# Performance work log

Hardware: AMD Instinct MI355X
Metric: run time of the kernel (lower is better)

Reference implementation:

```python
import jax, jax.numpy as jnp
import numpy as np
import math

D_MODEL = 1024
N_HEADS = 16
D_K = D_MODEL // N_HEADS
B, T = 4, 2048


def setup_inputs() -> dict:
    key = jax.random.key(0)
    ks = jax.random.split(key, 5)
    s = 1.0 / math.sqrt(D_MODEL)
    return {
        "x": jax.random.normal(ks[0], (B, T, D_MODEL), dtype=jnp.float32),
        "W_qkv": jax.random.normal(ks[1], (3 * D_MODEL, D_MODEL), dtype=jnp.float32) * s,
        "b_qkv": jax.random.normal(ks[2], (3 * D_MODEL,), dtype=jnp.float32) * 0.01,
        "W_out": jax.random.normal(ks[3], (D_MODEL, D_MODEL), dtype=jnp.float32) * s,
        "b_out": jax.random.normal(ks[4], (D_MODEL,), dtype=jnp.float32) * 0.01,
    }


def reference(x, W_qkv, b_qkv, W_out, b_out):
    Bn, Tn, C = x.shape
    # qkv projection: [B,T,3C]
    qkv = jnp.einsum("btc,oc->bto", x, W_qkv) + b_qkv
    # NOTE: original reshapes to (B,T,H,3*d_k) THEN chunks -> per-head interleaved layout
    qkv = qkv.reshape(Bn, Tn, N_HEADS, 3 * D_K).transpose(0, 2, 1, 3)  # [B,H,T,3dk]
    q, k, v = jnp.split(qkv, 3, axis=-1)  # each [B,H,T,dk]
    scores = jnp.einsum("bhtd,bhsd->bhts", q, k) / math.sqrt(D_K)
    causal = jnp.tril(jnp.ones((Tn, Tn), dtype=bool))
    scores = jnp.where(causal[None, None], scores, -jnp.inf)
    attn = jax.nn.softmax(scores, axis=-1)
    ctx = jnp.einsum("bhts,bhsd->bhtd", attn, v)  # [B,H,T,dk]
    ctx = ctx.transpose(0, 2, 1, 3).reshape(Bn, Tn, C)
    return jnp.einsum("btc,oc->bto", ctx, W_out) + b_out
```

## Files before the change

### kernel.cpp

```cpp
#include <hip/hip_runtime.h>

typedef __attribute__((ext_vector_type(8))) short short8;
typedef __attribute__((ext_vector_type(4))) float f32x4;
typedef __attribute__((ext_vector_type(16))) float f32x16;
typedef __attribute__((ext_vector_type(4))) unsigned int u32x4;
typedef __attribute__((ext_vector_type(4))) unsigned short u16x4;
typedef unsigned int u32;
typedef unsigned short u16;

#define DEV static __device__ __forceinline__

DEV u16 f2bf(float f) {
  union { float f; u32 u; } c; c.f = f;
  u32 r = (c.u + 0x7fffu + ((c.u >> 16) & 1u)) >> 16;
  return (u16)r;
}
DEV float bf2f(u16 v) {
  union { u32 u; float f; } c; c.u = ((u32)v) << 16;
  return c.f;
}
DEV short8 pack8(float4 a, float4 b) {
  short8 r;
  r[0]=(short)f2bf(a.x); r[1]=(short)f2bf(a.y); r[2]=(short)f2bf(a.z); r[3]=(short)f2bf(a.w);
  r[4]=(short)f2bf(b.x); r[5]=(short)f2bf(b.y); r[6]=(short)f2bf(b.z); r[7]=(short)f2bf(b.w);
  return r;
}
DEV u32 cvtpk(float lo, float hi) {
  u32 r;
  asm("v_cvt_pk_bf16_f32 %0, %1, %2" : "=v"(r) : "v"(lo), "v"(hi));
  return r;
}

#if __has_builtin(__builtin_amdgcn_exp2f)
DEV float fexp2(float x) { return __builtin_amdgcn_exp2f(x); }
#else
DEV float fexp2(float x) { return exp2f(x); }
#endif

DEV void glds16(const void* g, void* l) {
  __builtin_amdgcn_global_load_lds((const __attribute__((address_space(1))) u32*)g,
                                   (__attribute__((address_space(3))) u32*)l, 16, 0, 0);
}

DEV f32x16 mfma32(short8 a, short8 b, f32x16 c) {
  return __builtin_amdgcn_mfma_f32_32x32x16_bf16(a, b, c, 0, 0, 0);
}

constexpr int CDIM = 1024, TT = 2048, NH = 16, DK = 64;
#define QSC 0.1803368801111601f

__global__ void conv_bf16(const float* __restrict__ X, const float* __restrict__ W1,
                          const float* __restrict__ W2, u16* __restrict__ Xb,
                          u16* __restrict__ W1b, u16* __restrict__ W2b) {
  const long n0 = 1048576, n1 = 393216, n2 = 131072;
  for (long i = (long)blockIdx.x * blockDim.x + threadIdx.x; i < n0 + n1 + n2;
       i += (long)gridDim.x * blockDim.x) {
    const float* s; u16* d; long j = i;
    if (j < n0) { s = X; d = Xb; }
    else if (j < n0 + n1) { j -= n0; s = W1; d = W1b; }
    else { j -= n0 + n1; s = W2; d = W2b; }
    float4 a = ((const float4*)s)[2 * j];
    float4 b = ((const float4*)s)[2 * j + 1];
    ((short8*)d)[j] = pack8(a, b);
  }
}

__global__ void __launch_bounds__(512, 2)
qkv_gemm5(const u16* __restrict__ A, const u16* __restrict__ B,
          const float* __restrict__ bias, u16* __restrict__ Qb,
          u16* __restrict__ Kb, u16* __restrict__ VTb) {
  __shared__ u16 LS[3][3][128][64];
  const int tid = threadIdx.x, lane = tid & 63, wid = tid >> 6;
  const int lo = lane & 15, lg = lane >> 4;
  const int wm = wid >> 1, wn = wid & 1;
  const int rin = lane >> 3, blk = lane & 7;
  const int m0 = blockIdx.x * 256, n0 = blockIdx.y * 128;
  const int r7 = lo & 7;

  const u16* gA = A + (size_t)(m0 + wid * 16 + rin) * CDIM + (blk ^ rin) * 8;
  const u16* gB = B + (size_t)(n0 + wid * 16 + rin) * CDIM + (blk ^ rin) * 8;
  u16* lsb = &LS[0][0][wid * 16][0];

#define STGH0(bufi, kt)                                          \
  {                                                              \
    const int k0e = (kt) * 64;                                   \
    u16* lb = lsb + (bufi) * 24576;                              \
    glds16(gA + k0e, lb);                                        \
    glds16(gA + k0e + 8 * CDIM, lb + 512);                       \
    glds16(gB + k0e, lb + 16384);                                \
  }
#define STGH1(bufi, kt)                                          \
  {                                                              \
    const int k0e = (kt) * 64;                                   \
    u16* lb = lsb + (bufi) * 24576;                              \
    glds16(gA + k0e + 128 * CDIM, lb + 8192);                    \
    glds16(gA + k0e + 136 * CDIM, lb + 8704);                    \
    glds16(gB + k0e + 8 * CDIM, lb + 16896);                     \
  }

  f32x4 acc[4][4];
  const f32x4 fz = {0.f, 0.f, 0.f, 0.f};
#pragma unroll
  for (int i = 0; i < 4; ++i)
#pragma unroll
    for (int j = 0; j < 4; ++j) acc[i][j] = fz;

  STGH0(0, 0); STGH1(0, 0);
  STGH0(1, 1); STGH1(1, 1);
  asm volatile("s_waitcnt vmcnt(6)" ::: "memory");
  __builtin_amdgcn_s_barrier();

  int b0 = 0, b1 = 1, b2 = 2;
  for (int T = 0; T < 16; ++T) {
    const u16* pA = &LS[b0][wm >> 1][(wm & 1) * 64][0];
    const u16* pB = &LS[b0][2][wn * 64][0];
    short8 af[4], bfr[4];
#pragma unroll
    for (int mi = 0; mi < 4; ++mi)
      af[mi] = *(const short8*)&pA[(mi * 16 + lo) * 64 + ((lg ^ r7) * 8)];
#pragma unroll
    for (int ni = 0; ni < 4; ++ni)
      bfr[ni] = *(const short8*)&pB[(ni * 16 + lo) * 64 + ((lg ^ r7) * 8)];
    if (T < 14) STGH0(b2, T + 2);
    __builtin_amdgcn_sched_barrier(0);
    __builtin_amdgcn_s_barrier();
    asm volatile("s_waitcnt lgkmcnt(0)" ::: "memory");
    __builtin_amdgcn_sched_barrier(0);
    __builtin_amdgcn_s_setprio(1);
#pragma unroll
    for (int mi = 0; mi < 4; ++mi)
#pragma unroll
      for (int ni = 0; ni < 4; ++ni)
        acc[mi][ni] = __builtin_amdgcn_mfma_f32_16x16x32_bf16(af[mi], bfr[ni], acc[mi][ni], 0, 0, 0);
    __builtin_amdgcn_s_setprio(0);
    __builtin_amdgcn_sched_barrier(0);
    __builtin_amdgcn_s_barrier();
#pragma unroll
    for (int mi = 0; mi < 4; ++mi)
      af[mi] = *(const short8*)&pA[(mi * 16 + lo) * 64 + (((4 + lg) ^ r7) * 8)];
#pragma unroll
    for (int ni = 0; ni < 4; ++ni)
      bfr[ni] = *(const short8*)&pB[(ni * 16 + lo) * 64 + (((4 + lg) ^ r7) * 8)];
    if (T < 14) STGH1(b2, T + 2);
    __builtin_amdgcn_sched_barrier(0);
    if (T < 14) {
      asm volatile("s_waitcnt vmcnt(6)" ::: "memory");
    } else if (T == 14) {
      asm volatile("s_waitcnt vmcnt(0)" ::: "memory");
    }
    __builtin_amdgcn_s_barrier();
    asm volatile("s_waitcnt lgkmcnt(0)" ::: "memory");
    __builtin_amdgcn_sched_barrier(0);
    __builtin_amdgcn_s_setprio(1);
#pragma unroll
    for (int mi = 0; mi < 4; ++mi)
#pragma unroll
      for (int ni = 0; ni < 4; ++ni)
        acc[mi][ni] = __builtin_amdgcn_mfma_f32_16x16x32_bf16(af[mi], bfr[ni], acc[mi][ni], 0, 0, 0);
    __builtin_amdgcn_s_setprio(0);
    __builtin_amdgcn_sched_barrier(0);
    __builtin_amdgcn_s_barrier();
    const int tmp = b0; b0 = b1; b1 = b2; b2 = tmp;
  }
#undef STGH0
#undef STGH1

#pragma unroll
  for (int ni = 0; ni < 4; ++ni) {
    const int o = n0 + wn * 64 + ni * 16 + lo;
    const float bv = bias[o];
    const int hh = o / 192, rem = o - hh * 192, which = rem >> 6, d = rem & 63;
#pragma unroll
    for (int mi = 0; mi < 4; ++mi) {
      const int mb = m0 + wm * 64 + mi * 16 + lg * 4;
      const int bbi = mb >> 11, t0 = mb & 2047;
      const int bh = bbi * NH + hh;
      if (which == 2) {
        u16x4 pk;
#pragma unroll
        for (int r = 0; r < 4; ++r) pk[r] = f2bf(acc[mi][ni][r] + bv);
        *(u16x4*)&VTb[((size_t)bh * DK + d) * TT + t0] = pk;
      } else if (which == 1) {
#pragma unroll
        for (int r = 0; r < 4; ++r)
          Kb[((size_t)bh * TT + t0 + r) * DK + d] = f2bf(acc[mi][ni][r] + bv);
      } else {
#pragma unroll
        for (int r = 0; r < 4; ++r)
          Qb[((size_t)bh * TT + t0 + r) * DK + d] = f2bf((acc[mi][ni][r] + bv) * QSC);
      }
    }
  }
}

__global__ void __launch_bounds__(256, 4)
attn10(const u16* __restrict__ Qb, const u16* __restrict__ Kb,
       const u16* __restrict__ VTb, u16* __restrict__ PA, u16* __restrict__ PB,
       float* __restrict__ ML) {
  __shared__ u16 Kls[2][64][64];
  __shared__ u16 Vls[2][64][64];
  const int tid = threadIdx.x, lane = tid & 63, wv = tid >> 6;
  const int lq = lane & 31, h = lane >> 5;
  const int id = blockIdx.x;
  const int w = (id & 7) * 128 + (id >> 3);
  const int bh = w >> 4;
  const int pj = w & 7;
  const int sp = (w >> 3) & 1;
  const int bb = bh >> 4, head = bh & 15;
  const u16* Qp = Qb + (size_t)bh * TT * DK;
  const u16* Kp = Kb + (size_t)bh * TT * DK;
  const u16* Vp = VTb + (size_t)bh * DK * TT;
  const int rin = lane >> 3, blk = lane & 7;
  u16* PO = sp ? PB : PA;

  const u16* kga = Kp + (size_t)(wv * 16 + rin) * DK + (blk ^ rin) * 8;
  const u16* vga = Vp + (size_t)(wv * 16 + rin) * TT + (blk ^ rin) * 8;
  u16* kls0 = &Kls[0][wv * 16][0];
  u16* vls0 = &Vls[0][wv * 16][0];
  const int lds_half = 64 * 64;

#define STAGE10(bufi, kvt_)                                                 \
  {                                                                         \
    const int o_ = (bufi) * lds_half;                                       \
    glds16(kga + (size_t)(kvt_) * 4096, kls0 + o_);                         \
    glds16(kga + (size_t)(kvt_) * 4096 + 512, kls0 + o_ + 512);             \
    glds16(vga + (size_t)(kvt_) * 64, vls0 + o_);                           \
    glds16(vga + (size_t)(kvt_) * 64 + 8 * TT, vls0 + o_ + 512);            \
  }

  for (int pi = 0; pi < 2; ++pi) {
    const int qtile = pi ? (15 - pj) : pj;
    const int q0w = qtile * 128 + wv * 32;
    const int qrow = q0w + lq;

    short8 qw[4];
#pragma unroll
    for (int kk = 0; kk < 4; ++kk)
      qw[kk] = *(const short8*)&Qp[(size_t)qrow * DK + kk * 16 + h * 8];

    f32x16 oa0, oa1;
#pragma unroll
    for (int r = 0; r < 16; ++r) { oa0[r] = 0.f; oa1[r] = 0.f; }
    float l_s = 0.f;

    const int nt = 2 * qtile + 2;
    STAGE10(0, sp);
    __syncthreads();
    int buf = 0;
    for (int kvt = sp; kvt < nt; kvt += 2) {
      const int kv0 = kvt * 64;
      if (kvt + 2 < nt) STAGE10(buf ^ 1, kvt + 2);
      if (kv0 <= q0w + 31) {
        f32x16 s0, s1;
#pragma unroll
        for (int r = 0; r < 16; ++r) { s0[r] = 0.f; s1[r] = 0.f; }
        __builtin_amdgcn_s_setprio(1);
#pragma unroll
        for (int kk = 0; kk < 4; ++kk) {
          const short8 kf0 = *(const short8*)&Kls[buf][lq][(((2 * kk + h) ^ (lq & 7)) * 8)];
          const short8 kf1 = *(const short8*)&Kls[buf][32 + lq][(((2 * kk + h) ^ (lq & 7)) * 8)];
          s0 = mfma32(kf0, qw[kk], s0);
          s1 = mfma32(kf1, qw[kk], s1);
        }
        __builtin_amdgcn_s_setprio(0);
        const bool diag = (kv0 + 63 > q0w);
        if (diag) {
          const int lim = qrow - kv0 - 4 * h;
#pragma unroll
          for (int r = 0; r < 16; ++r) {
            const int kl = (r & 3) + 8 * (r >> 2);
            s0[r] = (kl <= lim) ? s0[r] : -1e30f;
            s1[r] = (kl + 32 <= lim) ? s1[r] : -1e30f;
          }
        }
        float rsa = 0.f, rsb = 0.f, rsc = 0.f, rsd = 0.f;
#pragma unroll
        for (int r = 0; r < 16; r += 4) {
          const float a0 = fexp2(s0[r]),     a1 = fexp2(s1[r]);
          const float b0 = fexp2(s0[r + 1]), b1 = fexp2(s1[r + 1]);
          const float c0 = fexp2(s0[r + 2]), c1 = fexp2(s1[r + 2]);
          const float d0 = fexp2(s0[r + 3]), d1 = fexp2(s1[r + 3]);
          s0[r] = a0; s1[r] = a1; s0[r + 1] = b0; s1[r + 1] = b1;
          s0[r + 2] = c0; s1[r + 2] = c1; s0[r + 3] = d0; s1[r + 3] = d1;
          rsa += a0 + a1; rsb += b0 + b1; rsc += c0 + c1; rsd += d0 + d1;
        }
        float rs = (rsa + rsb) + (rsc + rsd);
        rs += __shfl_xor(rs, 32);
        l_s += rs;
#pragma unroll
        for (int s = 0; s < 2; ++s) {
          u32 C[8];
#pragma unroll
          for (int j = 0; j < 8; ++j)
            C[j] = s ? cvtpk(s1[2 * j], s1[2 * j + 1]) : cvtpk(s0[2 * j], s0[2 * j + 1]);
#pragma unroll
          for (int b = 0; b < 2; ++b) {
            const int o = 4 * b;
            const u32 D1 = h ? C[o + 0] : C[o + 2];
            const u32 D2 = h ? C[o + 1] : C[o + 3];
            const u32 R1 = __shfl_xor(D1, 32);
            const u32 R2 = __shfl_xor(D2, 32);
            union { u32x4 w; short8 s8; } pa;
            pa.w[0] = h ? R1 : C[o + 0];
            pa.w[1] = h ? R2 : C[o + 1];
            pa.w[2] = h ? C[o + 2] : R1;
            pa.w[3] = h ? C[o + 3] : R2;
            const int ks = 2 * s + b;
            const short8 vb0 = *(const short8*)&Vls[buf][lq][(((2 * ks + h) ^ (lq & 7)) * 8)];
            const short8 vb1 = *(const short8*)&Vls[buf][32 + lq][(((2 * ks + h) ^ (lq & 7)) * 8)];
            __builtin_amdgcn_s_setprio(1);
            oa0 = mfma32(pa.s8, vb0, oa0);
            oa1 = mfma32(pa.s8, vb1, oa1);
            __builtin_amdgcn_s_setprio(0);
          }
        }
      }
      __syncthreads();
      buf ^= 1;
    }

#pragma unroll
    for (int r = 0; r < 16; ++r) {
      const int t = q0w + (r & 3) + 8 * (r >> 2) + 4 * h;
      const size_t rowb = ((size_t)(bb * TT + t)) * CDIM + head * DK;
      PO[rowb + lq] = f2bf(oa0[r]);
      PO[rowb + 32 + lq] = f2bf(oa1[r]);
    }
    if (h == 0) ML[((size_t)(sp * 64 + bh) << 11) + qrow] = l_s;
    __syncthreads();
  }
#undef STAGE10
}

__global__ void attn_merge(const u16* PA, const u16* PB,
                           const float* __restrict__ ML, u16* Ctx) {
  const int row = blockIdx.x;
  const int b = row >> 11, t = row & 2047;
  const int c = threadIdx.x * 4;
  const int head = c >> 6;
  const int bh = b * NH + head;
  const float lA = ML[((size_t)bh << 11) + t];
  const float lB = ML[((size_t)(64 + bh) << 11) + t];
  const float il = 1.0f / (lA + lB);
  const size_t idx = ((size_t)row) * CDIM + c;
  u16x4 pa = *(const u16x4*)&PA[idx];
  u16x4 pb = *(const u16x4*)&PB[idx];
  u16x4 o;
#pragma unroll
  for (int e = 0; e < 4; ++e) o[e] = f2bf((bf2f(pa[e]) + bf2f(pb[e])) * il);
  *(u16x4*)&Ctx[idx] = o;
}

__global__ void out_gemm2(const u16* __restrict__ A, const u16* __restrict__ B,
                          const float* __restrict__ bias, float* __restrict__ Out) {
  __shared__ u16 As[128][64];
  __shared__ u16 Bs[128][64];
  const int tid = threadIdx.x, lane = tid & 63, wv = tid >> 6;
  const int wr = wv >> 1, wc = wv & 1, lo = lane & 15, lg = lane >> 4;
  const int m0 = blockIdx.x * 128, n0 = blockIdx.y * 128;
  const int rin = lane >> 3, blk = lane & 7;

  f32x4 acc[4][4];
  const f32x4 fz = {0.f, 0.f, 0.f, 0.f};
#pragma unroll
  for (int i = 0; i < 4; ++i)
#pragma unroll
    for (int j = 0; j < 4; ++j) acc[i][j] = fz;

  for (int k0 = 0; k0 < CDIM; k0 += 64) {
    const u16* ga = A + (size_t)(m0 + 32 * wv + rin) * CDIM + k0 + blk * 8;
    const u16* gb = B + (size_t)(n0 + 32 * wv + rin) * CDIM + k0 + blk * 8;
#pragma unroll
    for (int i = 0; i < 4; ++i) glds16(ga + (size_t)(8 * i) * CDIM, &As[32 * wv + 8 * i][0]);
#pragma unroll
    for (int i = 0; i < 4; ++i) glds16(gb + (size_t)(8 * i) * CDIM, &Bs[32 * wv + 8 * i][0]);
    __syncthreads();
#pragma unroll
    for (int kk = 0; kk < 2; ++kk) {
      short8 af[4], bf[4];
#pragma unroll
      for (int mi = 0; mi < 4; ++mi) af[mi] = *(const short8*)&As[wr * 64 + mi * 16 + lo][kk * 32 + lg * 8];
#pragma unroll
      for (int ni = 0; ni < 4; ++ni) bf[ni] = *(const short8*)&Bs[wc * 64 + ni * 16 + lo][kk * 32 + lg * 8];
#pragma unroll
      for (int mi = 0; mi < 4; ++mi)
#pragma unroll
        for (int ni = 0; ni < 4; ++ni)
          acc[mi][ni] = __builtin_amdgcn_mfma_f32_16x16x32_bf16(af[mi], bf[ni], acc[mi][ni], 0, 0, 0);
    }
    __syncthreads();
  }

#pragma unroll
  for (int ni = 0; ni < 4; ++ni) {
    const int o = n0 + wc * 64 + ni * 16 + lo;
    const float bv = bias[o];
#pragma unroll
    for (int mi = 0; mi < 4; ++mi)
#pragma unroll
      for (int r = 0; r < 4; ++r)
        Out[(size_t)(m0 + wr * 64 + mi * 16 + lg * 4 + r) * CDIM + o] = acc[mi][ni][r] + bv;
  }
}

extern "C" void kernel_launch(void* const* d_in, const int* in_sizes, int n_in,
                              void* d_out, int out_size, void* d_ws, size_t ws_size,
                              hipStream_t stream) {
  const float* X = (const float*)d_in[0];
  const float* Wqkv = (const float*)d_in[1];
  const float* bqkv = (const float*)d_in[2];
  const float* Wout = (const float*)d_in[3];
  const float* bout = (const float*)d_in[4];
  float* Out = (float*)d_out;

  u16* Xb  = (u16*)d_ws;
  u16* W1b = Xb + 8388608;
  u16* W2b = W1b + 3145728;
  u16* Qb  = W2b + 1048576;
  u16* Kb  = Qb + 8388608;
  u16* VTb = Kb + 8388608;
  u16* Ctx = VTb + 8388608;

  conv_bf16<<<1024, 256, 0, stream>>>(X, Wqkv, Wout, Xb, W1b, W2b);
  qkv_gemm5<<<dim3(32, 24), 512, 0, stream>>>(Xb, W1b, bqkv, Qb, Kb, VTb);
  attn10<<<dim3(1024), 256, 0, stream>>>(Qb, Kb, VTb, Ctx, Xb, (float*)W1b);
  attn_merge<<<8192, 256, 0, stream>>>(Ctx, Xb, (const float*)W1b, Ctx);
  out_gemm2<<<dim3(64, 8), 256, 0, stream>>>(Ctx, W2b, bout, Out);
}
```

Baseline: 163.0 us.

## Widen QKV GEMM tile to 256x192 with double-buffered LDS

```diff
diff --git a/kernel.cpp b/kernel.cpp
--- a/kernel.cpp
+++ b/kernel.cpp
@@ -66,62 +66,63 @@
 }
 
 __global__ void __launch_bounds__(512, 2)
-qkv_gemm5(const u16* __restrict__ A, const u16* __restrict__ B,
+qkv_gemm6(const u16* __restrict__ A, const u16* __restrict__ B,
           const float* __restrict__ bias, u16* __restrict__ Qb,
           u16* __restrict__ Kb, u16* __restrict__ VTb) {
-  __shared__ u16 LS[3][3][128][64];
+  __shared__ u16 LSA[2][256][64];
+  __shared__ u16 LSB[2][192][64];
   const int tid = threadIdx.x, lane = tid & 63, wid = tid >> 6;
   const int lo = lane & 15, lg = lane >> 4;
-  const int wm = wid >> 1, wn = wid & 1;
+  const int wm = wid >> 2, wn = wid & 3;
   const int rin = lane >> 3, blk = lane & 7;
-  const int m0 = blockIdx.x * 256, n0 = blockIdx.y * 128;
+  const int m0 = blockIdx.x * 256, n0 = blockIdx.y * 192;
   const int r7 = lo & 7;
 
-  const u16* gA = A + (size_t)(m0 + wid * 16 + rin) * CDIM + (blk ^ rin) * 8;
-  const u16* gB = B + (size_t)(n0 + wid * 16 + rin) * CDIM + (blk ^ rin) * 8;
-  u16* lsb = &LS[0][0][wid * 16][0];
-
-#define STGH0(bufi, kt)                                          \
+  const u16* gA = A + (size_t)(m0 + wid * 32 + rin) * CDIM + (blk ^ rin) * 8;
+  const u16* gB = B + (size_t)(n0 + wid * 24 + rin) * CDIM + (blk ^ rin) * 8;
+  u16* lA0 = &LSA[0][wid * 32][0];
+  u16* lB0 = &LSB[0][wid * 24][0];
+
+#define STGA6(bufi, kt)                                          \
   {                                                              \
-    const int k0e = (kt) * 64;                                   \
-    u16* lb = lsb + (bufi) * 24576;                              \
-    glds16(gA + k0e, lb);                                        \
-    glds16(gA + k0e + 8 * CDIM, lb + 512);                       \
-    glds16(gB + k0e, lb + 16384);                                \
-  }
-#define STGH1(bufi, kt)                                          \
+    u16* la = lA0 + (bufi) * 16384;                              \
+    glds16(gA + (kt) * 64, la);                                  \
+    glds16(gA + (kt) * 64 + 8 * CDIM, la + 512);                 \
+    glds16(gA + (kt) * 64 + 16 * CDIM, la + 1024);               \
+    glds16(gA + (kt) * 64 + 24 * CDIM, la + 1536);               \
+  }
+#define STGB6(bufi, kt)                                          \
   {                                                              \
-    const int k0e = (kt) * 64;                                   \
-    u16* lb = lsb + (bufi) * 24576;                              \
-    glds16(gA + k0e + 128 * CDIM, lb + 8192);                    \
-    glds16(gA + k0e + 136 * CDIM, lb + 8704);                    \
-    glds16(gB + k0e + 8 * CDIM, lb + 16896);                     \
-  }
-
-  f32x4 acc[4][4];
+    u16* lb = lB0 + (bufi) * 12288;                              \
+    glds16(gB + (kt) * 64, lb);                                  \
+    glds16(gB + (kt) * 64 + 8 * CDIM, lb + 512);                 \
+    glds16(gB + (kt) * 64 + 16 * CDIM, lb + 1024);               \
+  }
+
+  f32x4 acc[8][3];
   const f32x4 fz = {0.f, 0.f, 0.f, 0.f};
 #pragma unroll
-  for (int i = 0; i < 4; ++i)
-#pragma unroll
-    for (int j = 0; j < 4; ++j) acc[i][j] = fz;
-
-  STGH0(0, 0); STGH1(0, 0);
-  STGH0(1, 1); STGH1(1, 1);
-  asm volatile("s_waitcnt vmcnt(6)" ::: "memory");
+  for (int i = 0; i < 8; ++i)
+#pragma unroll
+    for (int j = 0; j < 3; ++j) acc[i][j] = fz;
+
+  STGA6(0, 0);
+  STGB6(0, 0);
+  asm volatile("s_waitcnt vmcnt(0)" ::: "memory");
   __builtin_amdgcn_s_barrier();
 
-  int b0 = 0, b1 = 1, b2 = 2;
   for (int T = 0; T < 16; ++T) {
-    const u16* pA = &LS[b0][wm >> 1][(wm & 1) * 64][0];
-    const u16* pB = &LS[b0][2][wn * 64][0];
-    short8 af[4], bfr[4];
+    const int b = T & 1;
+    const u16* pA = &LSA[b][wm * 128][0];
+    const u16* pB = &LSB[b][wn * 48][0];
+    short8 af[4], bfr[3];
 #pragma unroll
     for (int mi = 0; mi < 4; ++mi)
       af[mi] = *(const short8*)&pA[(mi * 16 + lo) * 64 + ((lg ^ r7) * 8)];
 #pragma unroll
-    for (int ni = 0; ni < 4; ++ni)
+    for (int ni = 0; ni < 3; ++ni)
       bfr[ni] = *(const short8*)&pB[(ni * 16 + lo) * 64 + ((lg ^ r7) * 8)];
-    if (T < 14) STGH0(b2, T + 2);
+    if (T < 15) STGA6(b ^ 1, T + 1);
     __builtin_amdgcn_sched_barrier(0);
     __builtin_amdgcn_s_barrier();
     asm volatile("s_waitcnt lgkmcnt(0)" ::: "memory");
@@ -130,24 +131,35 @@
 #pragma unroll
     for (int mi = 0; mi < 4; ++mi)
 #pragma unroll
-      for (int ni = 0; ni < 4; ++ni)
+      for (int ni = 0; ni < 3; ++ni)
         acc[mi][ni] = __builtin_amdgcn_mfma_f32_16x16x32_bf16(af[mi], bfr[ni], acc[mi][ni], 0, 0, 0);
     __builtin_amdgcn_s_setprio(0);
     __builtin_amdgcn_sched_barrier(0);
     __builtin_amdgcn_s_barrier();
 #pragma unroll
     for (int mi = 0; mi < 4; ++mi)
+      af[mi] = *(const short8*)&pA[((mi + 4) * 16 + lo) * 64 + ((lg ^ r7) * 8)];
+    if (T < 15) STGB6(b ^ 1, T + 1);
+    __builtin_amdgcn_sched_barrier(0);
+    __builtin_amdgcn_s_barrier();
+    asm volatile("s_waitcnt lgkmcnt(0)" ::: "memory");
+    __builtin_amdgcn_sched_barrier(0);
+    __builtin_amdgcn_s_setprio(1);
+#pragma unroll
+    for (int mi = 0; mi < 4; ++mi)
+#pragma unroll
+      for (int ni = 0; ni < 3; ++ni)
+        acc[mi + 4][ni] = __builtin_amdgcn_mfma_f32_16x16x32_bf16(af[mi], bfr[ni], acc[mi + 4][ni], 0, 0, 0);
+    __builtin_amdgcn_s_setprio(0);
+    __builtin_amdgcn_sched_barrier(0);
+    __builtin_amdgcn_s_barrier();
+#pragma unroll
+    for (int mi = 0; mi < 4; ++mi)
       af[mi] = *(const short8*)&pA[(mi * 16 + lo) * 64 + (((4 + lg) ^ r7) * 8)];
 #pragma unroll
-    for (int ni = 0; ni < 4; ++ni)
+    for (int ni = 0; ni < 3; ++ni)
       bfr[ni] = *(const short8*)&pB[(ni * 16 + lo) * 64 + (((4 + lg) ^ r7) * 8)];
-    if (T < 14) STGH1(b2, T + 2);
-    __builtin_amdgcn_sched_barrier(0);
-    if (T < 14) {
-      asm volatile("s_waitcnt vmcnt(6)" ::: "memory");
-    } else if (T == 14) {
-      asm volatile("s_waitcnt vmcnt(0)" ::: "memory");
-    }
+    __builtin_amdgcn_sched_barrier(0);
     __builtin_amdgcn_s_barrier();
     asm volatile("s_waitcnt lgkmcnt(0)" ::: "memory");
     __builtin_amdgcn_sched_barrier(0);
@@ -155,24 +167,40 @@
 #pragma unroll
     for (int mi = 0; mi < 4; ++mi)
 #pragma unroll
-      for (int ni = 0; ni < 4; ++ni)
+      for (int ni = 0; ni < 3; ++ni)
         acc[mi][ni] = __builtin_amdgcn_mfma_f32_16x16x32_bf16(af[mi], bfr[ni], acc[mi][ni], 0, 0, 0);
     __builtin_amdgcn_s_setprio(0);
     __builtin_amdgcn_sched_barrier(0);
     __builtin_amdgcn_s_barrier();
-    const int tmp = b0; b0 = b1; b1 = b2; b2 = tmp;
-  }
-#undef STGH0
-#undef STGH1
-
-#pragma unroll
-  for (int ni = 0; ni < 4; ++ni) {
-    const int o = n0 + wn * 64 + ni * 16 + lo;
+#pragma unroll
+    for (int mi = 0; mi < 4; ++mi)
+      af[mi] = *(const short8*)&pA[((mi + 4) * 16 + lo) * 64 + (((4 + lg) ^ r7) * 8)];
+    __builtin_amdgcn_sched_barrier(0);
+    __builtin_amdgcn_s_barrier();
+    asm volatile("s_waitcnt lgkmcnt(0)" ::: "memory");
+    __builtin_amdgcn_sched_barrier(0);
+    __builtin_amdgcn_s_setprio(1);
+#pragma unroll
+    for (int mi = 0; mi < 4; ++mi)
+#pragma unroll
+      for (int ni = 0; ni < 3; ++ni)
+        acc[mi + 4][ni] = __builtin_amdgcn_mfma_f32_16x16x32_bf16(af[mi], bfr[ni], acc[mi + 4][ni], 0, 0, 0);
+    __builtin_amdgcn_s_setprio(0);
+    if (T < 15) asm volatile("s_waitcnt vmcnt(0)" ::: "memory");
+    __builtin_amdgcn_sched_barrier(0);
+    __builtin_amdgcn_s_barrier();
+  }
+#undef STGA6
+#undef STGB6
+
+#pragma unroll
+  for (int ni = 0; ni < 3; ++ni) {
+    const int o = n0 + wn * 48 + ni * 16 + lo;
     const float bv = bias[o];
     const int hh = o / 192, rem = o - hh * 192, which = rem >> 6, d = rem & 63;
 #pragma unroll
-    for (int mi = 0; mi < 4; ++mi) {
-      const int mb = m0 + wm * 64 + mi * 16 + lg * 4;
+    for (int mi = 0; mi < 8; ++mi) {
+      const int mb = m0 + wm * 128 + mi * 16 + lg * 4;
       const int bbi = mb >> 11, t0 = mb & 2047;
       const int bh = bbi * NH + hh;
       if (which == 2) {
@@ -422,7 +450,7 @@
   u16* Ctx = VTb + 8388608;
 
   conv_bf16<<<1024, 256, 0, stream>>>(X, Wqkv, Wout, Xb, W1b, W2b);
-  qkv_gemm5<<<dim3(32, 24), 512, 0, stream>>>(Xb, W1b, bqkv, Qb, Kb, VTb);
+  qkv_gemm6<<<dim3(32, 16), 512, 0, stream>>>(Xb, W1b, bqkv, Qb, Kb, VTb);
   attn10<<<dim3(1024), 256, 0, stream>>>(Qb, Kb, VTb, Ctx, Xb, (float*)W1b);
   attn_merge<<<8192, 256, 0, stream>>>(Ctx, Xb, (const float*)W1b, Ctx);
   out_gemm2<<<dim3(64, 8), 256, 0, stream>>>(Ctx, W2b, bout, Out);
```

After: 164.5 us. Within noise of the previous version (+0.9%).

## Fuse split-attention merge into output GEMM A-tile load with swizzled LDS

Applied to the files above, without the earlier changes.

```diff
diff --git a/kernel.cpp b/kernel.cpp
--- a/kernel.cpp
+++ b/kernel.cpp
@@ -332,26 +332,8 @@
 #undef STAGE10
 }
 
-__global__ void attn_merge(const u16* PA, const u16* PB,
-                           const float* __restrict__ ML, u16* Ctx) {
-  const int row = blockIdx.x;
-  const int b = row >> 11, t = row & 2047;
-  const int c = threadIdx.x * 4;
-  const int head = c >> 6;
-  const int bh = b * NH + head;
-  const float lA = ML[((size_t)bh << 11) + t];
-  const float lB = ML[((size_t)(64 + bh) << 11) + t];
-  const float il = 1.0f / (lA + lB);
-  const size_t idx = ((size_t)row) * CDIM + c;
-  u16x4 pa = *(const u16x4*)&PA[idx];
-  u16x4 pb = *(const u16x4*)&PB[idx];
-  u16x4 o;
-#pragma unroll
-  for (int e = 0; e < 4; ++e) o[e] = f2bf((bf2f(pa[e]) + bf2f(pb[e])) * il);
-  *(u16x4*)&Ctx[idx] = o;
-}
-
-__global__ void out_gemm2(const u16* __restrict__ A, const u16* __restrict__ B,
+__global__ void out_gemm3(const u16* __restrict__ PA, const u16* __restrict__ PB,
+                          const float* __restrict__ ML, const u16* __restrict__ B,
                           const float* __restrict__ bias, float* __restrict__ Out) {
   __shared__ u16 As[128][64];
   __shared__ u16 Bs[128][64];
@@ -359,6 +341,7 @@
   const int wr = wv >> 1, wc = wv & 1, lo = lane & 15, lg = lane >> 4;
   const int m0 = blockIdx.x * 128, n0 = blockIdx.y * 128;
   const int rin = lane >> 3, blk = lane & 7;
+  const int r7 = lo & 7;
 
   f32x4 acc[4][4];
   const f32x4 fz = {0.f, 0.f, 0.f, 0.f};
@@ -367,21 +350,44 @@
 #pragma unroll
     for (int j = 0; j < 4; ++j) acc[i][j] = fz;
 
-  for (int k0 = 0; k0 < CDIM; k0 += 64) {
-    const u16* ga = A + (size_t)(m0 + 32 * wv + rin) * CDIM + k0 + blk * 8;
-    const u16* gb = B + (size_t)(n0 + 32 * wv + rin) * CDIM + k0 + blk * 8;
-#pragma unroll
-    for (int i = 0; i < 4; ++i) glds16(ga + (size_t)(8 * i) * CDIM, &As[32 * wv + 8 * i][0]);
-#pragma unroll
-    for (int i = 0; i < 4; ++i) glds16(gb + (size_t)(8 * i) * CDIM, &Bs[32 * wv + 8 * i][0]);
+  const u16* gb = B + (size_t)(n0 + 32 * wv + rin) * CDIM + (blk ^ rin) * 8;
+
+  for (int kt = 0; kt < 16; ++kt) {
+    const int k0 = kt * 64;
+#pragma unroll
+    for (int i = 0; i < 4; ++i) {
+      const int row = 32 * wv + 8 * i + rin;
+      const int mg = m0 + row;
+      const int t = mg & 2047, bidx = mg >> 11;
+      const int bh = bidx * NH + kt;
+      const float lA = ML[((size_t)bh << 11) + t];
+      const float lB = ML[((size_t)(64 + bh) << 11) + t];
+      const float il = 1.0f / (lA + lB);
+      const size_t gi = (size_t)mg * CDIM + k0 + blk * 8;
+      const short8 pa = *(const short8*)&PA[gi];
+      const short8 pb = *(const short8*)&PB[gi];
+      float f[8];
+#pragma unroll
+      for (int e = 0; e < 8; ++e)
+        f[e] = (bf2f((u16)pa[e]) + bf2f((u16)pb[e])) * il;
+      union { u32x4 w; short8 s8; } v;
+#pragma unroll
+      for (int j = 0; j < 4; ++j) v.w[j] = cvtpk(f[2 * j], f[2 * j + 1]);
+      *(short8*)&As[row][(blk ^ rin) * 8] = v.s8;
+    }
+#pragma unroll
+    for (int i = 0; i < 4; ++i)
+      glds16(gb + k0 + (size_t)(8 * i) * CDIM, &Bs[32 * wv + 8 * i][0]);
     __syncthreads();
 #pragma unroll
     for (int kk = 0; kk < 2; ++kk) {
       short8 af[4], bf[4];
 #pragma unroll
-      for (int mi = 0; mi < 4; ++mi) af[mi] = *(const short8*)&As[wr * 64 + mi * 16 + lo][kk * 32 + lg * 8];
-#pragma unroll
-      for (int ni = 0; ni < 4; ++ni) bf[ni] = *(const short8*)&Bs[wc * 64 + ni * 16 + lo][kk * 32 + lg * 8];
+      for (int mi = 0; mi < 4; ++mi)
+        af[mi] = *(const short8*)&As[wr * 64 + mi * 16 + lo][(((kk * 4 + lg) ^ r7) * 8)];
+#pragma unroll
+      for (int ni = 0; ni < 4; ++ni)
+        bf[ni] = *(const short8*)&Bs[wc * 64 + ni * 16 + lo][(((kk * 4 + lg) ^ r7) * 8)];
 #pragma unroll
       for (int mi = 0; mi < 4; ++mi)
 #pragma unroll
@@ -424,6 +430,5 @@
   conv_bf16<<<1024, 256, 0, stream>>>(X, Wqkv, Wout, Xb, W1b, W2b);
   qkv_gemm5<<<dim3(32, 24), 512, 0, stream>>>(Xb, W1b, bqkv, Qb, Kb, VTb);
   attn10<<<dim3(1024), 256, 0, stream>>>(Qb, Kb, VTb, Ctx, Xb, (float*)W1b);
-  attn_merge<<<8192, 256, 0, stream>>>(Ctx, Xb, (const float*)W1b, Ctx);
-  out_gemm2<<<dim3(64, 8), 256, 0, stream>>>(Ctx, W2b, bout, Out);
-}
+  out_gemm3<<<dim3(64, 8), 256, 0, stream>>>(Ctx, Xb, (const float*)W1b, W2b, bout, Out);
+}
```

After: 185.2 us. +13.6%, slower.
